# Optimization experiments

Measured on AMD Instinct MI355X. Metric: run time of the kernel, lower is better.

## Reference

```python
import jax, jax.numpy as jnp
import numpy as np

B, N, D_IN, D_OUT = 4, 512, 128, 64
TEMP = 1.0
BN_EPS = 1e-5


def setup_inputs() -> dict:
    key = jax.random.key(0)
    ks = jax.random.split(key, 9)
    return {
        "x": jax.random.normal(ks[0], (B, N, D_IN), jnp.float32),
        "att_proj_w": jax.random.normal(ks[1], (D_OUT, D_IN), jnp.float32) * 0.08,
        "att_proj_b": jax.random.normal(ks[2], (D_OUT,), jnp.float32) * 0.01,
        "att_weight": jax.random.normal(ks[3], (D_OUT, 1), jnp.float32) * 0.15,
        "proj_with_att_w": jax.random.normal(ks[4], (D_OUT, D_IN), jnp.float32) * 0.08,
        "proj_with_att_b": jax.random.normal(ks[5], (D_OUT,), jnp.float32) * 0.01,
        "proj_without_att_w": jax.random.normal(ks[6], (D_OUT, D_IN), jnp.float32) * 0.08,
        "proj_without_att_b": jax.random.normal(ks[7], (D_OUT,), jnp.float32) * 0.01,
        "bn_gamma": jnp.ones((D_OUT,), jnp.float32),
        "bn_beta": jnp.zeros((D_OUT,), jnp.float32),
    }


def reference(x, att_proj_w, att_proj_b, att_weight,
              proj_with_att_w, proj_with_att_b,
              proj_without_att_w, proj_without_att_b,
              bn_gamma, bn_beta):
    # Dropout is identity (inference). Pairwise node multiplication: (B,N,N,D_in)
    pair = x[:, :, None, :] * x[:, None, :, :]
    # Linear + tanh on the pairwise tensor -> (B,N,N,D_out)
    a = jnp.tanh(jnp.einsum('bijd,od->bijo', pair, att_proj_w) + att_proj_b)
    # Score via learned vector, temperature, softmax over second node axis (torch dim=-2 of (B,N,N,1))
    scores = jnp.einsum('bijo,o->bij', a, att_weight[:, 0]) / TEMP
    att = jax.nn.softmax(scores, axis=2)  # normalize over j
    # Attention-weighted aggregation + two projections (torch Linear: x @ W.T + b)
    agg = jnp.einsum('bij,bjd->bid', att, x)
    h = (agg @ proj_with_att_w.T + proj_with_att_b) \
        + (x @ proj_without_att_w.T + proj_without_att_b)
    # BatchNorm1d (training-mode batch stats) over flattened (B*N, D_out)
    hf = h.reshape(-1, h.shape[-1])
    mean = hf.mean(axis=0)
    var = hf.var(axis=0)  # biased, as torch BN uses for normalization
    y = (hf - mean) / jnp.sqrt(var + BN_EPS) * bn_gamma + bn_beta
    y = y.reshape(h.shape)
    return jax.nn.selu(y)
```

## Files before the change

kernel.cpp:

```cpp
#include <hip/hip_runtime.h>
#include <math.h>

#define NB 4
#define NN 512
#define DIN 128
#define DOUT 64
#define TI 2
#define CHROWS 32
#define NCHL 8
#define NTOT (NB * NN)

typedef __attribute__((ext_vector_type(8))) short short8;
typedef __attribute__((ext_vector_type(8))) unsigned short ushort8;
typedef __attribute__((ext_vector_type(16))) float f32x16;

__device__ __forceinline__ unsigned short f2bf(float f) {
    union { float f; unsigned u; } v; v.f = f;
    unsigned r = v.u + 0x7fffu + ((v.u >> 16) & 1u);
    return (unsigned short)(r >> 16);
}

__device__ __forceinline__ float bf2f(unsigned short u) {
    union { unsigned u; float f; } v; v.u = ((unsigned)u) << 16; return v.f;
}

__global__ void x_to_bf16(const float* __restrict__ x, unsigned short* __restrict__ xbf) {
    const int idx = blockIdx.x * 256 + threadIdx.x;
    float4 v = ((const float4*)x)[idx];
    ushort4 o;
    o.x = f2bf(v.x); o.y = f2bf(v.y); o.z = f2bf(v.z); o.w = f2bf(v.w);
    ((ushort4*)xbf)[idx] = o;
}

__global__ __launch_bounds__(256, 3) void gat_main(
    const float* __restrict__ x,
    const unsigned short* __restrict__ xbf,
    const float* __restrict__ apw,
    const float* __restrict__ apb,
    const float* __restrict__ attw,
    float* __restrict__ pnum,
    float* __restrict__ pden)
{
    __shared__ unsigned short xt[2][CHROWS * DIN];
    __shared__ float scp[2][TI][256];
    __shared__ float xis[TI][DIN];
    __shared__ float red_s[4][TI];

    float* pagg = (float*)&xt[0][0];

    const int t = threadIdx.x;
    const int blk = blockIdx.x;
    const int jh = blk & 1;
    const int rp = blk >> 1;
    const int b = rp >> 8;
    const int rowbase = (rp & 255) * TI;
    const int rid0 = rp * TI;
    const float* xb = x + (size_t)b * NN * DIN;
    const unsigned short* xbb = xbf + (size_t)b * NN * DIN;

    {
        const int i = t >> 7, d = t & 127;
        xis[i][d] = xb[(size_t)(rowbase + i) * DIN + d];
    }

    const int lane = t & 63, wid = t >> 6;
    const int qi = wid & 1;
    const int oh = wid >> 1;
    const int l31 = lane & 31;
    const int hi = lane >> 5;

    const int r0 = t >> 4, g0 = t & 15;
    const int st_off0 = r0 * 256 + ((g0 ^ (r0 & 7)) << 4);
    const int r1 = 16 + r0;
    const int st_off1 = r1 * 256 + ((g0 ^ (r1 & 7)) << 4);

    int rdoff[8];
    #pragma unroll
    for (int ks = 0; ks < 8; ++ks)
        rdoff[ks] = l31 * 256 + (((ks * 2 + hi) ^ (l31 & 7)) << 4);

    ushort8 v0a = ((const ushort8*)xbb)[(jh * NCHL) * 512 + t];
    ushort8 v0b = ((const ushort8*)xbb)[(jh * NCHL) * 512 + t + 256];
    __syncthreads();

    short8 afr[8];
    {
        const float* wrow = apw + (size_t)(oh * 32 + l31) * DIN;
        const float* xk0 = &xis[qi][0];
        #pragma unroll
        for (int ks = 0; ks < 8; ++ks) {
            const int k0 = ks * 16 + hi * 8;
            float4 w0 = *(const float4*)(wrow + k0);
            float4 w1 = *(const float4*)(wrow + k0 + 4);
            const float* xk = xk0 + k0;
            short8 fr;
            fr[0] = (short)f2bf(w0.x * xk[0]);
            fr[1] = (short)f2bf(w0.y * xk[1]);
            fr[2] = (short)f2bf(w0.z * xk[2]);
            fr[3] = (short)f2bf(w0.w * xk[3]);
            fr[4] = (short)f2bf(w1.x * xk[4]);
            fr[5] = (short)f2bf(w1.y * xk[5]);
            fr[6] = (short)f2bf(w1.z * xk[6]);
            fr[7] = (short)f2bf(w1.w * xk[7]);
            afr[ks] = fr;
        }
    }

    const float C2 = 2.885390081777927f;
    float awm2[16], abc[16], sumw = 0.0f;
    #pragma unroll
    for (int r = 0; r < 16; ++r) {
        const int crow = (r & 3) + 8 * (r >> 2) + 4 * hi;
        const int o = oh * 32 + crow;
        float wv = attw[o], bv = apb[o];
        awm2[r] = -2.0f * wv;
        abc[r] = bv * C2;
        sumw += wv;
    }

    *(ushort8*)((char*)&xt[0][0] + st_off0) = v0a;
    *(ushort8*)((char*)&xt[0][0] + st_off1) = v0b;
    __syncthreads();

    f32x16 accA, accB;
    ushort8 nva, nvb;

#define COMPUTE(ACC, BUF) do {                                                  \
    f32x16 zz_ = {0.f,0.f,0.f,0.f,0.f,0.f,0.f,0.f,                              \
                  0.f,0.f,0.f,0.f,0.f,0.f,0.f,0.f};                             \
    ACC = zz_;                                                                  \
    _Pragma("unroll")                                                           \
    for (int ks_ = 0; ks_ < 8; ++ks_) {                                         \
        short8 bk_ = *(const short8*)((const char*)&xt[BUF][0] + rdoff[ks_]);   \
        ACC = __builtin_amdgcn_mfma_f32_32x32x16_bf16(afr[ks_], bk_, ACC, 0, 0, 0); \
    }                                                                           \
} while (0)

#define POST(ACC, CH) do {                                                      \
    float sp_ = sumw;                                                           \
    _Pragma("unroll")                                                           \
    for (int r_ = 0; r_ < 16; ++r_) {                                           \
        float arg_ = fmaf(ACC[r_], C2, abc[r_]);                                \
        float u_, rc_;                                                          \
        asm("v_exp_f32 %0, %1" : "=v"(u_) : "v"(arg_));                         \
        float den_ = u_ + 1.0f;                                                 \
        asm("v_rcp_f32 %0, %1" : "=v"(rc_) : "v"(den_));                        \
        sp_ = fmaf(awm2[r_], rc_, sp_);                                         \
    }                                                                           \
    sp_ += __shfl_xor(sp_, 32);                                                 \
    if (lane < 32) scp[oh][qi][(CH) * 32 + l31] = sp_;                          \
} while (0)

#define LOADR(CH) do {                                                          \
    nva = ((const ushort8*)xbb)[(jh * NCHL + (CH)) * 512 + t];                  \
    nvb = ((const ushort8*)xbb)[(jh * NCHL + (CH)) * 512 + t + 256];            \
} while (0)

#define WRITES(BUF) do {                                                        \
    *(ushort8*)((char*)&xt[BUF][0] + st_off0) = nva;                            \
    *(ushort8*)((char*)&xt[BUF][0] + st_off1) = nvb;                            \
} while (0)

    LOADR(1);
    COMPUTE(accA, 0);
    WRITES(1);
    __syncthreads();
    for (int cb = 1; cb <= NCHL - 3; cb += 2) {
        LOADR(cb + 1);
        COMPUTE(accB, 1);
        POST(accA, cb - 1);
        WRITES(0);
        __syncthreads();
        LOADR(cb + 2);
        COMPUTE(accA, 0);
        POST(accB, cb);
        WRITES(1);
        __syncthreads();
    }
    COMPUTE(accB, 1);
    POST(accA, NCHL - 2);
    POST(accB, NCHL - 1);
    __syncthreads();

    {
        float s0 = scp[0][0][t] + scp[1][0][t];
        float s1 = scp[0][1][t] + scp[1][1][t];
        float e0 = __expf(s0), e1 = __expf(s1);
        scp[0][0][t] = e0;
        scp[0][1][t] = e1;
        float ss0 = e0, ss1 = e1;
        #pragma unroll
        for (int m = 1; m < 64; m <<= 1) {
            ss0 += __shfl_xor(ss0, m);
            ss1 += __shfl_xor(ss1, m);
        }
        if (lane == 0) { red_s[wid][0] = ss0; red_s[wid][1] = ss1; }
    }
    __syncthreads();
    if (t < TI) {
        float den = red_s[0][t] + red_s[1][t] + red_s[2][t] + red_s[3][t];
        pden[jh * NTOT + rid0 + t] = den;
    }

    const float* esc0 = &scp[0][0][0];
    const float* esc1 = &scp[0][1][0];
    {
        const int d0 = (t & 31) * 4, q = t >> 5;
        const unsigned short* xc = xbb + (size_t)(jh * 256) * DIN + d0;
        float a0[4] = {0.f, 0.f, 0.f, 0.f};
        float a1[4] = {0.f, 0.f, 0.f, 0.f};
        #pragma unroll 4
        for (int jj = q * 32; jj < q * 32 + 32; ++jj) {
            ushort4 xv = *(const ushort4*)(xc + (size_t)jj * DIN);
            float e0v = esc0[jj], e1v = esc1[jj];
            float x0 = bf2f(xv.x), x1 = bf2f(xv.y);
            float x2 = bf2f(xv.z), x3 = bf2f(xv.w);
            a0[0] = fmaf(e0v, x0, a0[0]); a0[1] = fmaf(e0v, x1, a0[1]);
            a0[2] = fmaf(e0v, x2, a0[2]); a0[3] = fmaf(e0v, x3, a0[3]);
            a1[0] = fmaf(e1v, x0, a1[0]); a1[1] = fmaf(e1v, x1, a1[1]);
            a1[2] = fmaf(e1v, x2, a1[2]); a1[3] = fmaf(e1v, x3, a1[3]);
        }
        #pragma unroll
        for (int c = 0; c < 4; ++c) {
            pagg[(q * TI + 0) * DIN + d0 + c] = a0[c];
            pagg[(q * TI + 1) * DIN + d0 + c] = a1[c];
        }
    }
    __syncthreads();
    {
        const int i = t >> 7, d = t & 127;
        float s = 0.f;
        #pragma unroll
        for (int q = 0; q < 8; ++q) s += pagg[(q * TI + i) * DIN + d];
        pnum[(size_t)(jh * NTOT + rid0 + i) * DIN + d] = s;
    }
#undef COMPUTE
#undef POST
#undef LOADR
#undef WRITES
}

__global__ __launch_bounds__(256, 2) void combine_proj(
    const float* __restrict__ x,
    const float* __restrict__ pnum, const float* __restrict__ pden,
    const float* __restrict__ pww, const float* __restrict__ pwb,
    const float* __restrict__ pow_, const float* __restrict__ pob,
    float* __restrict__ out)
{
    __shared__ float wL[DOUT][DIN + 1];
    __shared__ float vL[16][DIN];
    __shared__ float invL[16];

    const int t = threadIdx.x;
    const int rbase = blockIdx.x * 16;
    const int o = t & 63, rq = t >> 6;

    for (int k = t; k < DOUT * DIN; k += 256) wL[k >> 7][k & 127] = pww[k];
    for (int k = t; k < 16 * DIN; k += 256) {
        const int i = k >> 7, d = k & 127;
        const int r = rbase + i;
        vL[i][d] = pnum[(size_t)r * DIN + d] + pnum[(size_t)(NTOT + r) * DIN + d];
    }
    if (t < 16) {
        const int r = rbase + t;
        invL[t] = 1.0f / (pden[r] + pden[NTOT + r]);
    }
    __syncthreads();

    float accp[4] = {0.f, 0.f, 0.f, 0.f};
    #pragma unroll 4
    for (int d = 0; d < DIN; ++d) {
        float w = wL[o][d];
        #pragma unroll
        for (int rr = 0; rr < 4; ++rr)
            accp[rr] = fmaf(w, vL[rq + rr * 4][d], accp[rr]);
    }
    __syncthreads();

    for (int k = t; k < DOUT * DIN; k += 256) wL[k >> 7][k & 127] = pow_[k];
    for (int k = t; k < 16 * DIN; k += 256) {
        const int i = k >> 7, d = k & 127;
        vL[i][d] = x[(size_t)(rbase + i) * DIN + d];
    }
    __syncthreads();

    float res[4] = {0.f, 0.f, 0.f, 0.f};
    #pragma unroll 4
    for (int d = 0; d < DIN; ++d) {
        float w = wL[o][d];
        #pragma unroll
        for (int rr = 0; rr < 4; ++rr)
            res[rr] = fmaf(w, vL[rq + rr * 4][d], res[rr]);
    }
    const float bias = pwb[o] + pob[o];
    #pragma unroll
    for (int rr = 0; rr < 4; ++rr) {
        const int i = rq + rr * 4;
        out[(size_t)(rbase + i) * DOUT + o] = accp[rr] * invL[i] + res[rr] + bias;
    }
}

__global__ void bn_stats(const float* __restrict__ h, float* __restrict__ stats) {
    const int c = blockIdx.x;
    const int t = threadIdx.x;
    float s = 0.f, s2 = 0.f;
    for (int r = t; r < NTOT; r += 256) {
        float v = h[(size_t)r * DOUT + c];
        s += v; s2 += v * v;
    }
    __shared__ float rs[256], rs2[256];
    rs[t] = s; rs2[t] = s2;
    __syncthreads();
    for (int k = 128; k > 0; k >>= 1) {
        if (t < k) { rs[t] += rs[t + k]; rs2[t] += rs2[t + k]; }
        __syncthreads();
    }
    if (t == 0) {
        const float inv_n = 1.0f / (float)NTOT;
        float mean = rs[0] * inv_n;
        float var = rs2[0] * inv_n - mean * mean;
        stats[c] = mean;
        stats[DOUT + c] = rsqrtf(var + 1e-5f);
    }
}

__global__ void bn_selu(float* __restrict__ out, const float* __restrict__ stats,
                        const float* __restrict__ gamma, const float* __restrict__ beta) {
    const int idx = blockIdx.x * 256 + threadIdx.x;
    const int c = idx & 63;
    float v = out[idx];
    float y = (v - stats[c]) * stats[DOUT + c] * gamma[c] + beta[c];
    const float scale = 1.0507009873554805f;
    const float alpha = 1.6732632423543772f;
    out[idx] = y > 0.0f ? scale * y : scale * alpha * (__expf(y) - 1.0f);
}

extern "C" void kernel_launch(void* const* d_in, const int* in_sizes, int n_in,
                              void* d_out, int out_size, void* d_ws, size_t ws_size,
                              hipStream_t stream) {
    const float* x    = (const float*)d_in[0];
    const float* apw  = (const float*)d_in[1];
    const float* apb  = (const float*)d_in[2];
    const float* attw = (const float*)d_in[3];
    const float* pww  = (const float*)d_in[4];
    const float* pwb  = (const float*)d_in[5];
    const float* pow_ = (const float*)d_in[6];
    const float* pob  = (const float*)d_in[7];
    const float* gmm  = (const float*)d_in[8];
    const float* bta  = (const float*)d_in[9];
    float* out = (float*)d_out;

    char* ws = (char*)d_ws;
    float* stats = (float*)ws;
    unsigned short* xbf = (unsigned short*)(ws + 1024);
    float* pnum = (float*)(ws + 528384);
    float* pden = (float*)(ws + 528384 + 2097152);

    x_to_bf16<<<256, 256, 0, stream>>>(x, xbf);
    gat_main<<<2 * NTOT / TI, 256, 0, stream>>>(x, xbf, apw, apb, attw, pnum, pden);
    combine_proj<<<NTOT / 16, 256, 0, stream>>>(x, pnum, pden, pww, pwb, pow_, pob, out);
    bn_stats<<<DOUT, 256, 0, stream>>>(out, stats);
    bn_selu<<<(NTOT * DOUT) / 256, 256, 0, stream>>>(out, stats, gmm, bta);
}
```

Before: 71.26 us.

## Double chunk size in attention pipeline and fuse BN stats into projection

The main attention kernel now stages 64-row chunks (4 chunks instead of 8), which halves the number of barriers and lets two MFMA tiles be computed per stage with the softmax-score post-processing interleaved. Separately, the BN statistics kernel is removed: each combine_proj block writes per-channel partial sums, and the last block (found with an atomic counter reset in x_to_bf16) reduces them into mean and rstd. This saves one kernel launch and a full reread of the output. In exchange it doubles the shared-memory staging buffer, which may lower occupancy, and adds threadfence and atomic synchronisation.

```diff
diff --git a/kernel.cpp b/kernel.cpp
--- a/kernel.cpp
+++ b/kernel.cpp
@@ -6,8 +6,8 @@
 #define DIN 128
 #define DOUT 64
 #define TI 2
-#define CHROWS 32
-#define NCHL 8
+#define CHROWS 64
+#define NCHL 4
 #define NTOT (NB * NN)
 
 typedef __attribute__((ext_vector_type(8))) short short8;
@@ -24,8 +24,10 @@
     union { unsigned u; float f; } v; v.u = ((unsigned)u) << 16; return v.f;
 }
 
-__global__ void x_to_bf16(const float* __restrict__ x, unsigned short* __restrict__ xbf) {
+__global__ void x_to_bf16(const float* __restrict__ x, unsigned short* __restrict__ xbf,
+                          int* __restrict__ cnt) {
     const int idx = blockIdx.x * 256 + threadIdx.x;
+    if (idx == 0) cnt[0] = 0;
     float4 v = ((const float4*)x)[idx];
     ushort4 o;
     o.x = f2bf(v.x); o.y = f2bf(v.y); o.z = f2bf(v.z); o.w = f2bf(v.w);
@@ -71,16 +73,17 @@
 
     const int r0 = t >> 4, g0 = t & 15;
     const int st_off0 = r0 * 256 + ((g0 ^ (r0 & 7)) << 4);
-    const int r1 = 16 + r0;
-    const int st_off1 = r1 * 256 + ((g0 ^ (r1 & 7)) << 4);
 
     int rdoff[8];
     #pragma unroll
     for (int ks = 0; ks < 8; ++ks)
         rdoff[ks] = l31 * 256 + (((ks * 2 + hi) ^ (l31 & 7)) << 4);
 
-    ushort8 v0a = ((const ushort8*)xbb)[(jh * NCHL) * 512 + t];
-    ushort8 v0b = ((const ushort8*)xbb)[(jh * NCHL) * 512 + t + 256];
+    const ushort8* gsrc = (const ushort8*)xbb + (size_t)jh * 4096;
+    ushort8 nv0 = gsrc[t];
+    ushort8 nv1 = gsrc[256 + t];
+    ushort8 nv2 = gsrc[512 + t];
+    ushort8 nv3 = gsrc[768 + t];
     __syncthreads();
 
     short8 afr[8];
@@ -118,25 +121,33 @@
         sumw += wv;
     }
 
-    *(ushort8*)((char*)&xt[0][0] + st_off0) = v0a;
-    *(ushort8*)((char*)&xt[0][0] + st_off1) = v0b;
-    __syncthreads();
-
-    f32x16 accA, accB;
-    ushort8 nva, nvb;
-
-#define COMPUTE(ACC, BUF) do {                                                  \
+#define WRITES(BUF) do {                                                        \
+    *(ushort8*)((char*)&xt[BUF][0] + st_off0) = nv0;                            \
+    *(ushort8*)((char*)&xt[BUF][0] + st_off0 + 4096) = nv1;                     \
+    *(ushort8*)((char*)&xt[BUF][0] + st_off0 + 8192) = nv2;                     \
+    *(ushort8*)((char*)&xt[BUF][0] + st_off0 + 12288) = nv3;                    \
+} while (0)
+
+#define LOADR(CH) do {                                                          \
+    nv0 = gsrc[(CH) * 1024 + t];                                                \
+    nv1 = gsrc[(CH) * 1024 + 256 + t];                                          \
+    nv2 = gsrc[(CH) * 1024 + 512 + t];                                          \
+    nv3 = gsrc[(CH) * 1024 + 768 + t];                                          \
+} while (0)
+
+#define COMPUTE(ACC, BUF, S) do {                                               \
     f32x16 zz_ = {0.f,0.f,0.f,0.f,0.f,0.f,0.f,0.f,                              \
                   0.f,0.f,0.f,0.f,0.f,0.f,0.f,0.f};                             \
     ACC = zz_;                                                                  \
     _Pragma("unroll")                                                           \
     for (int ks_ = 0; ks_ < 8; ++ks_) {                                         \
-        short8 bk_ = *(const short8*)((const char*)&xt[BUF][0] + rdoff[ks_]);   \
+        short8 bk_ = *(const short8*)((const char*)&xt[BUF][0] +                \
+                                      rdoff[ks_] + (S) * 8192);                 \
         ACC = __builtin_amdgcn_mfma_f32_32x32x16_bf16(afr[ks_], bk_, ACC, 0, 0, 0); \
     }                                                                           \
 } while (0)
 
-#define POST(ACC, CH) do {                                                      \
+#define POST(ACC, I32) do {                                                     \
     float sp_ = sumw;                                                           \
     _Pragma("unroll")                                                           \
     for (int r_ = 0; r_ < 16; ++r_) {                                           \
@@ -148,38 +159,42 @@
         sp_ = fmaf(awm2[r_], rc_, sp_);                                         \
     }                                                                           \
     sp_ += __shfl_xor(sp_, 32);                                                 \
-    if (lane < 32) scp[oh][qi][(CH) * 32 + l31] = sp_;                          \
+    if (lane < 32) scp[oh][qi][(I32) * 32 + l31] = sp_;                         \
 } while (0)
 
-#define LOADR(CH) do {                                                          \
-    nva = ((const ushort8*)xbb)[(jh * NCHL + (CH)) * 512 + t];                  \
-    nvb = ((const ushort8*)xbb)[(jh * NCHL + (CH)) * 512 + t + 256];            \
-} while (0)
-
-#define WRITES(BUF) do {                                                        \
-    *(ushort8*)((char*)&xt[BUF][0] + st_off0) = nva;                            \
-    *(ushort8*)((char*)&xt[BUF][0] + st_off1) = nvb;                            \
-} while (0)
+    f32x16 a0, a1, p1;
+
+    WRITES(0);
+    __syncthreads();
 
     LOADR(1);
-    COMPUTE(accA, 0);
+    COMPUTE(a0, 0, 0);
+    COMPUTE(a1, 0, 1);
+    POST(a0, 0);
     WRITES(1);
     __syncthreads();
-    for (int cb = 1; cb <= NCHL - 3; cb += 2) {
-        LOADR(cb + 1);
-        COMPUTE(accB, 1);
-        POST(accA, cb - 1);
-        WRITES(0);
-        __syncthreads();
-        LOADR(cb + 2);
-        COMPUTE(accA, 0);
-        POST(accB, cb);
-        WRITES(1);
-        __syncthreads();
-    }
-    COMPUTE(accB, 1);
-    POST(accA, NCHL - 2);
-    POST(accB, NCHL - 1);
+    p1 = a1;
+    LOADR(2);
+    COMPUTE(a0, 1, 0);
+    POST(p1, 1);
+    COMPUTE(a1, 1, 1);
+    POST(a0, 2);
+    WRITES(0);
+    __syncthreads();
+    p1 = a1;
+    LOADR(3);
+    COMPUTE(a0, 0, 0);
+    POST(p1, 3);
+    COMPUTE(a1, 0, 1);
+    POST(a0, 4);
+    WRITES(1);
+    __syncthreads();
+    p1 = a1;
+    COMPUTE(a0, 1, 0);
+    POST(p1, 5);
+    COMPUTE(a1, 1, 1);
+    POST(a0, 6);
+    POST(a1, 7);
     __syncthreads();
 
     {
@@ -207,23 +222,23 @@
     {
         const int d0 = (t & 31) * 4, q = t >> 5;
         const unsigned short* xc = xbb + (size_t)(jh * 256) * DIN + d0;
-        float a0[4] = {0.f, 0.f, 0.f, 0.f};
-        float a1[4] = {0.f, 0.f, 0.f, 0.f};
+        float b0[4] = {0.f, 0.f, 0.f, 0.f};
+        float b1[4] = {0.f, 0.f, 0.f, 0.f};
         #pragma unroll 4
         for (int jj = q * 32; jj < q * 32 + 32; ++jj) {
             ushort4 xv = *(const ushort4*)(xc + (size_t)jj * DIN);
             float e0v = esc0[jj], e1v = esc1[jj];
             float x0 = bf2f(xv.x), x1 = bf2f(xv.y);
             float x2 = bf2f(xv.z), x3 = bf2f(xv.w);
-            a0[0] = fmaf(e0v, x0, a0[0]); a0[1] = fmaf(e0v, x1, a0[1]);
-            a0[2] = fmaf(e0v, x2, a0[2]); a0[3] = fmaf(e0v, x3, a0[3]);
-            a1[0] = fmaf(e1v, x0, a1[0]); a1[1] = fmaf(e1v, x1, a1[1]);
-            a1[2] = fmaf(e1v, x2, a1[2]); a1[3] = fmaf(e1v, x3, a1[3]);
+            b0[0] = fmaf(e0v, x0, b0[0]); b0[1] = fmaf(e0v, x1, b0[1]);
+            b0[2] = fmaf(e0v, x2, b0[2]); b0[3] = fmaf(e0v, x3, b0[3]);
+            b1[0] = fmaf(e1v, x0, b1[0]); b1[1] = fmaf(e1v, x1, b1[1]);
+            b1[2] = fmaf(e1v, x2, b1[2]); b1[3] = fmaf(e1v, x3, b1[3]);
         }
         #pragma unroll
         for (int c = 0; c < 4; ++c) {
-            pagg[(q * TI + 0) * DIN + d0 + c] = a0[c];
-            pagg[(q * TI + 1) * DIN + d0 + c] = a1[c];
+            pagg[(q * TI + 0) * DIN + d0 + c] = b0[c];
+            pagg[(q * TI + 1) * DIN + d0 + c] = b1[c];
         }
     }
     __syncthreads();
@@ -245,11 +260,15 @@
     const float* __restrict__ pnum, const float* __restrict__ pden,
     const float* __restrict__ pww, const float* __restrict__ pwb,
     const float* __restrict__ pow_, const float* __restrict__ pob,
-    float* __restrict__ out)
+    float* __restrict__ out, float* __restrict__ pbn,
+    int* __restrict__ cnt, float* __restrict__ stats)
 {
     __shared__ float wL[DOUT][DIN + 1];
     __shared__ float vL[16][DIN];
     __shared__ float invL[16];
+    __shared__ float psum[4][DOUT];
+    __shared__ float psum2[4][DOUT];
+    __shared__ int isLast;
 
     const int t = threadIdx.x;
     const int rbase = blockIdx.x * 16;
@@ -293,34 +312,51 @@
             res[rr] = fmaf(w, vL[rq + rr * 4][d], res[rr]);
     }
     const float bias = pwb[o] + pob[o];
+    float ls = 0.f, ls2 = 0.f;
     #pragma unroll
     for (int rr = 0; rr < 4; ++rr) {
         const int i = rq + rr * 4;
-        out[(size_t)(rbase + i) * DOUT + o] = accp[rr] * invL[i] + res[rr] + bias;
-    }
-}
-
-__global__ void bn_stats(const float* __restrict__ h, float* __restrict__ stats) {
-    const int c = blockIdx.x;
-    const int t = threadIdx.x;
-    float s = 0.f, s2 = 0.f;
-    for (int r = t; r < NTOT; r += 256) {
-        float v = h[(size_t)r * DOUT + c];
-        s += v; s2 += v * v;
-    }
-    __shared__ float rs[256], rs2[256];
-    rs[t] = s; rs2[t] = s2;
-    __syncthreads();
-    for (int k = 128; k > 0; k >>= 1) {
-        if (t < k) { rs[t] += rs[t + k]; rs2[t] += rs2[t + k]; }
-        __syncthreads();
-    }
+        float h = accp[rr] * invL[i] + res[rr] + bias;
+        out[(size_t)(rbase + i) * DOUT + o] = h;
+        ls += h; ls2 += h * h;
+    }
+    psum[rq][o] = ls;
+    psum2[rq][o] = ls2;
+    __syncthreads();
+    if (t < DOUT) {
+        pbn[((size_t)blockIdx.x * 2 + 0) * DOUT + t] =
+            psum[0][t] + psum[1][t] + psum[2][t] + psum[3][t];
+        pbn[((size_t)blockIdx.x * 2 + 1) * DOUT + t] =
+            psum2[0][t] + psum2[1][t] + psum2[2][t] + psum2[3][t];
+    }
+    __threadfence();
     if (t == 0) {
+        int v = atomicAdd(cnt, 1);
+        isLast = (v == (int)gridDim.x - 1);
+    }
+    __syncthreads();
+    if (!isLast) return;
+    __threadfence();
+
+    {
+        const int c = t & 63, grp = t >> 6;
+        float s = 0.f, s2 = 0.f;
+        for (int bb = grp * 32; bb < grp * 32 + 32; ++bb) {
+            s += pbn[((size_t)bb * 2 + 0) * DOUT + c];
+            s2 += pbn[((size_t)bb * 2 + 1) * DOUT + c];
+        }
+        psum[grp][c] = s;
+        psum2[grp][c] = s2;
+    }
+    __syncthreads();
+    if (t < DOUT) {
         const float inv_n = 1.0f / (float)NTOT;
-        float mean = rs[0] * inv_n;
-        float var = rs2[0] * inv_n - mean * mean;
-        stats[c] = mean;
-        stats[DOUT + c] = rsqrtf(var + 1e-5f);
+        float s = psum[0][t] + psum[1][t] + psum[2][t] + psum[3][t];
+        float s2 = psum2[0][t] + psum2[1][t] + psum2[2][t] + psum2[3][t];
+        float mean = s * inv_n;
+        float var = s2 * inv_n - mean * mean;
+        stats[t] = mean;
+        stats[DOUT + t] = rsqrtf(var + 1e-5f);
     }
 }
 
@@ -352,13 +388,15 @@
 
     char* ws = (char*)d_ws;
     float* stats = (float*)ws;
+    int* cnt = (int*)(ws + 512);
     unsigned short* xbf = (unsigned short*)(ws + 1024);
     float* pnum = (float*)(ws + 528384);
     float* pden = (float*)(ws + 528384 + 2097152);
-
-    x_to_bf16<<<256, 256, 0, stream>>>(x, xbf);
+    float* pbn  = (float*)(ws + 528384 + 2097152 + 16384);
+
+    x_to_bf16<<<256, 256, 0, stream>>>(x, xbf, cnt);
     gat_main<<<2 * NTOT / TI, 256, 0, stream>>>(x, xbf, apw, apb, attw, pnum, pden);
-    combine_proj<<<NTOT / 16, 256, 0, stream>>>(x, pnum, pden, pww, pwb, pow_, pob, out);
-    bn_stats<<<DOUT, 256, 0, stream>>>(out, stats);
+    combine_proj<<<NTOT / 16, 256, 0, stream>>>(x, pnum, pden, pww, pwb, pow_, pob,
+                                                out, pbn, cnt, stats);
     bn_selu<<<(NTOT * DOUT) / 256, 256, 0, stream>>>(out, stats, gmm, bta);
 }
```

New measurement: 77.19 us. 1.08x slower.
